# Kernel tuning notes

Measured on AMD Instinct MI355X. Metric: run time of the kernel, lower is better.

The kernel has to match this reference:

```python
import jax, jax.numpy as jnp
import numpy as np

B, S, H = 4, 2048, 768
NUM_POS = B * (S // 4)  # fixed count of positive clc_label entries (2048, even)
NEG_BIG = -1000000000.0


def setup_inputs() -> dict:
    key = jax.random.key(0)
    k1, k2, k3, k4, k5 = jax.random.split(key, 5)
    encoded_states = jax.random.normal(k1, (B, S, H), dtype=jnp.float32)
    # sorted cell-ids -> contiguous segments for the equality mask
    indicator = jnp.sort(jax.random.randint(k2, (B, S), 0, 256, dtype=jnp.int32), axis=-1)
    # clc_label: first S//4 positions per row are positive targets (class ids in [1,S)),
    # last S//2 positions are -1 (attendable keys), rest 0 (ignored)
    pos_labels = jax.random.randint(k3, (B, S // 4), 1, S, dtype=jnp.int32)
    clc_label = jnp.zeros((B, S), dtype=jnp.int32)
    clc_label = clc_label.at[:, : S // 4].set(pos_labels)
    clc_label = clc_label.at[:, S // 2:].set(-1)
    # uniform_linear params (torch Linear: y = x @ W.T + b)
    W = jax.random.normal(k4, (H, H), dtype=jnp.float32) / np.sqrt(H)
    b = jax.random.normal(k5, (H,), dtype=jnp.float32) * 0.01
    return {"encoded_states": encoded_states, "W": W, "b": b,
            "indicator": indicator, "clc_label": clc_label}


def _ce(logits, labels):
    # mean cross entropy; all labels are > 0 here so ignore_index=0 never triggers
    logp = jax.nn.log_softmax(logits, axis=-1)
    return -jnp.take_along_axis(logp, labels[:, None], axis=1).mean()


def reference(encoded_states, W, b, indicator, clc_label):
    # indicator-equality mask matmul == within-segment sum (the segment-reduce emulation)
    seg_mask = (indicator[:, :, None] == indicator[:, None, :]).astype(encoded_states.dtype)  # [B,S,S]
    agg = jnp.einsum("bij,bjh->bih", seg_mask, encoded_states)  # [B,S,H]
    # Q and K use the SAME linear on the same input -> compute once
    proj = jnp.tanh(agg @ W.T + b)  # [B,S,H]
    scores = jnp.einsum("bih,bjh->bij", proj, proj)  # [B,S,S]
    # attend only to positions where clc_label < 0
    allow = (clc_label < 0)[:, None, :]  # [B,1,S]
    scores = scores + jnp.where(allow, 0.0, NEG_BIG).astype(scores.dtype)
    flat = scores.reshape(-1, S)          # [B*S, S]
    labels = clc_label.reshape(-1)        # [B*S]
    pos_idx = jnp.nonzero(labels > 0, size=NUM_POS)[0]  # row-major order == torch bool-indexing
    logits = flat[pos_idx]                # [NUM_POS, S]
    labs = labels[pos_idx]                # [NUM_POS]
    sep_logits, sep_labels = logits[0::2], labs[0::2]
    tok_logits, tok_labels = logits[1::2], labs[1::2]
    sep_loss = _ce(sep_logits, sep_labels)
    tok_loss = _ce(tok_logits, tok_labels)
    sep_correct = jnp.sum((jnp.argmax(sep_logits, axis=-1).astype(jnp.int32) == sep_labels).astype(jnp.float32))
    tok_correct = jnp.sum((jnp.argmax(tok_logits, axis=-1).astype(jnp.int32) == tok_labels).astype(jnp.float32))
    sep_count = jnp.asarray(sep_logits.shape[0] + 1e-6, dtype=jnp.float32)
    tok_count = jnp.asarray(tok_logits.shape[0] + 1e-6, dtype=jnp.float32)
    return ((sep_loss, sep_correct, sep_count), (tok_loss, tok_correct, tok_count))
```

## Files before the change

kernel.cpp:

```cpp
#include <hip/hip_runtime.h>
#include <math.h>
#include <limits.h>

#define BB 4
#define SS 2048
#define HH 768
#define MAXSEG 256
#define NUM_POS (BB*(SS/4))
#define NEG_BIG -1000000000.0f

typedef _Float16 f16x8 __attribute__((ext_vector_type(8)));
typedef _Float16 f16x4 __attribute__((ext_vector_type(4)));
typedef float    f32x4 __attribute__((ext_vector_type(4)));

__global__ __launch_bounds__(256) void k_scanW(
    const int* __restrict__ ind, const int* __restrict__ clc,
    const float* __restrict__ W, _Float16* __restrict__ Wh,
    int* __restrict__ seg_id, int* __restrict__ seg_start,
    int* __restrict__ nseg, int* __restrict__ pos_local, int* __restrict__ pos_cnt,
    int* __restrict__ allowCnt, int* __restrict__ firstAllow)
{
  int t = threadIdx.x;
  if (blockIdx.x >= BB) {
    int idx = (blockIdx.x - BB)*256 + t;
    float4 v = ((const float4*)W)[idx];
    f16x4 h;
    h[0] = (_Float16)v.x; h[1] = (_Float16)v.y;
    h[2] = (_Float16)v.z; h[3] = (_Float16)v.w;
    *(f16x4*)(Wh + (size_t)idx*4) = h;
    return;
  }
  int b = blockIdx.x;
  int lane = t & 63, wid = t >> 6;
  __shared__ int sInd[SS];
  __shared__ int sWave[4];
  __shared__ int sAC[MAXSEG];
  __shared__ int sFA[MAXSEG];
  for (int i = t; i < SS; i += 256) sInd[i] = ind[b*SS + i];
  sAC[t] = 0; sFA[t] = INT_MAX;
  __syncthreads();

  int i0 = t * 8;
  int f[8], cv[8];
  int lsum = 0;
  #pragma unroll
  for (int u = 0; u < 8; u++) {
    int i = i0 + u;
    f[u] = (i == 0) ? 0 : (sInd[i] != sInd[i-1]);
    cv[u] = clc[b*SS + i];
    lsum += f[u];
  }
  int x = lsum;
  #pragma unroll
  for (int off = 1; off < 64; off <<= 1) {
    int v = __shfl_up(x, off, 64);
    if (lane >= off) x += v;
  }
  if (lane == 63) sWave[wid] = x;
  __syncthreads();
  int base = 0;
  for (int w = 0; w < wid; w++) base += sWave[w];
  int run = base + x - lsum;
  int rid[8];
  #pragma unroll
  for (int u = 0; u < 8; u++) {
    int i = i0 + u;
    run += f[u];
    rid[u] = run;
    seg_id[b*SS + i] = run;
    if (f[u] || i == 0) seg_start[b*(MAXSEG+1) + run] = i;
  }
  if (t == 255) { nseg[b] = run + 1; seg_start[b*(MAXSEG+1) + run + 1] = SS; }

  #pragma unroll
  for (int u = 0; u < 8; u++) {
    if (cv[u] < 0) {
      atomicAdd(&sAC[rid[u]], 1);
      atomicMin(&sFA[rid[u]], i0 + u);
    }
  }
  __syncthreads();
  allowCnt[b*MAXSEG + t]   = sAC[t];
  firstAllow[b*MAXSEG + t] = sFA[t];

  int psum = 0;
  int p[8];
  #pragma unroll
  for (int u = 0; u < 8; u++) { p[u] = (cv[u] > 0) ? 1 : 0; psum += p[u]; }
  x = psum;
  #pragma unroll
  for (int off = 1; off < 64; off <<= 1) {
    int v = __shfl_up(x, off, 64);
    if (lane >= off) x += v;
  }
  __syncthreads();
  if (lane == 63) sWave[wid] = x;
  __syncthreads();
  base = 0;
  for (int w = 0; w < wid; w++) base += sWave[w];
  int rank = base + x - psum;
  #pragma unroll
  for (int u = 0; u < 8; u++) {
    if (p[u]) { pos_local[b*SS + rank] = i0 + u; rank++; }
  }
  if (t == 255) pos_cnt[b] = rank;
}

__global__ __launch_bounds__(1024) void k_segsum(
    const float* __restrict__ es,
    const int* __restrict__ seg_start, const int* __restrict__ nseg,
    _Float16* __restrict__ segsum_h)
{
  __shared__ float sP[4][HH];
  int blk = blockIdx.x, t = threadIdx.x;
  int b = blk >> 8, s = blk & 255;
  _Float16* o = segsum_h + ((size_t)b*MAXSEG + s)*HH;
  if (s >= nseg[b]) {
    if (t < HH) o[t] = (_Float16)0.f;
    return;
  }
  int g = t >> 8, tt = t & 255;
  int st = seg_start[b*(MAXSEG+1) + s];
  int en = seg_start[b*(MAXSEG+1) + s + 1];
  int len = en - st;
  int q = (len + 3) >> 2;
  int gs = st + g*q;
  int ge = gs + q; if (ge > en) ge = en;
  const float* base = es + (size_t)b*SS*HH;
  float a0 = 0.f, a1 = 0.f, a2 = 0.f;
  float b0 = 0.f, b1 = 0.f, b2 = 0.f;
  float c0 = 0.f, c1 = 0.f, c2 = 0.f;
  float d0 = 0.f, d1 = 0.f, d2 = 0.f;
  int i = gs;
  for (; i + 4 <= ge; i += 4) {
    const float* r0 = base + (size_t)i*HH;
    const float* r1 = r0 + HH;
    const float* r2 = r1 + HH;
    const float* r3 = r2 + HH;
    a0 += r0[tt]; a1 += r0[tt+256]; a2 += r0[tt+512];
    b0 += r1[tt]; b1 += r1[tt+256]; b2 += r1[tt+512];
    c0 += r2[tt]; c1 += r2[tt+256]; c2 += r2[tt+512];
    d0 += r3[tt]; d1 += r3[tt+256]; d2 += r3[tt+512];
  }
  for (; i < ge; i++) {
    const float* r = base + (size_t)i*HH;
    a0 += r[tt]; a1 += r[tt+256]; a2 += r[tt+512];
  }
  sP[g][tt]     = (a0 + b0) + (c0 + d0);
  sP[g][tt+256] = (a1 + b1) + (c1 + d1);
  sP[g][tt+512] = (a2 + b2) + (c2 + d2);
  __syncthreads();
  if (t < HH) {
    float v = (sP[0][t] + sP[1][t]) + (sP[2][t] + sP[3][t]);
    o[t] = (_Float16)v;
  }
}

__global__ __launch_bounds__(192) void k_gemmU(
    const _Float16* __restrict__ Ah, const _Float16* __restrict__ Wh,
    const float* __restrict__ bias, _Float16* __restrict__ Uh)
{
  int tid = threadIdx.x;
  int w = tid >> 6, lane = tid & 63;
  int tile = blockIdx.x*3 + w;
  int tm = tile / 24, tn = tile % 24;
  int rb = tm*32, cb = tn*32;
  int m0 = lane & 15, quad = lane >> 4;
  const _Float16* A0 = Ah + (size_t)(rb + m0)*HH + quad*8;
  const _Float16* A1 = A0 + (size_t)16*HH;
  const _Float16* B0 = Wh + (size_t)(cb + m0)*HH + quad*8;
  const _Float16* B1 = B0 + (size_t)16*HH;
  f32x4 acc00 = {0.f,0.f,0.f,0.f}, acc01 = {0.f,0.f,0.f,0.f};
  f32x4 acc10 = {0.f,0.f,0.f,0.f}, acc11 = {0.f,0.f,0.f,0.f};
  #pragma unroll 4
  for (int k0 = 0; k0 < HH; k0 += 32) {
    f16x8 a0 = *(const f16x8*)(A0 + k0);
    f16x8 a1 = *(const f16x8*)(A1 + k0);
    f16x8 b0 = *(const f16x8*)(B0 + k0);
    f16x8 b1 = *(const f16x8*)(B1 + k0);
    acc00 = __builtin_amdgcn_mfma_f32_16x16x32_f16(a0, b0, acc00, 0, 0, 0);
    acc01 = __builtin_amdgcn_mfma_f32_16x16x32_f16(a0, b1, acc01, 0, 0, 0);
    acc10 = __builtin_amdgcn_mfma_f32_16x16x32_f16(a1, b0, acc10, 0, 0, 0);
    acc11 = __builtin_amdgcn_mfma_f32_16x16x32_f16(a1, b1, acc11, 0, 0, 0);
  }
  float bc0 = bias[cb + m0], bc1 = bias[cb + 16 + m0];
  int r0 = rb + quad*4;
  #pragma unroll
  for (int i = 0; i < 4; i++) {
    Uh[(size_t)(r0+i)*HH    + cb + m0]      = (_Float16)tanhf(acc00[i] + bc0);
    Uh[(size_t)(r0+i)*HH    + cb + 16 + m0] = (_Float16)tanhf(acc01[i] + bc1);
    Uh[(size_t)(r0+16+i)*HH + cb + m0]      = (_Float16)tanhf(acc10[i] + bc0);
    Uh[(size_t)(r0+16+i)*HH + cb + 16 + m0] = (_Float16)tanhf(acc11[i] + bc1);
  }
}

__global__ __launch_bounds__(256) void k_gram(
    const _Float16* __restrict__ Uh, float* __restrict__ G)
{
  int tid = threadIdx.x;
  int w = tid >> 6, lane = tid & 63;
  int tile = blockIdx.x*4 + w;
  int b = tile >> 8, rem = tile & 255;
  int rb = (rem >> 4)*16, cb = (rem & 15)*16;
  int m0 = lane & 15, quad = lane >> 4;
  const _Float16* Ub = Uh + (size_t)b*MAXSEG*HH;
  const _Float16* A0 = Ub + (size_t)(rb + m0)*HH + quad*8;
  const _Float16* B0 = Ub + (size_t)(cb + m0)*HH + quad*8;
  f32x4 acc = {0.f,0.f,0.f,0.f};
  #pragma unroll 4
  for (int k0 = 0; k0 < HH; k0 += 32) {
    f16x8 a  = *(const f16x8*)(A0 + k0);
    f16x8 bb = *(const f16x8*)(B0 + k0);
    acc = __builtin_amdgcn_mfma_f32_16x16x32_f16(a, bb, acc, 0, 0, 0);
  }
  float* Gb = G + (size_t)b*MAXSEG*MAXSEG;
  int r0 = rb + quad*4;
  #pragma unroll
  for (int i = 0; i < 4; i++)
    Gb[(size_t)(r0+i)*MAXSEG + cb + m0] = acc[i];
}

__global__ __launch_bounds__(256) void k_seglse(
    const float* __restrict__ G, const int* __restrict__ allowCnt,
    const int* __restrict__ firstAllow, const int* __restrict__ nseg,
    float* __restrict__ lse, int* __restrict__ amax)
{
  int lane = threadIdx.x & 63, wid = threadIdx.x >> 6;
  int row = blockIdx.x * 4 + wid;
  int b = row >> 8, si = row & 255;
  if (si >= nseg[b]) return;
  const float* g = G + ((size_t)b*MAXSEG + si)*MAXSEG;
  const int* ac = allowCnt + b*MAXSEG;
  const int* fa = firstAllow + b*MAXSEG;

  float4 gv = ((const float4*)g)[lane];
  int4   av = ((const int4*)ac)[lane];
  int4   fv = ((const int4*)fa)[lane];
  float gvv[4] = {gv.x, gv.y, gv.z, gv.w};
  int   avv[4] = {av.x, av.y, av.z, av.w};
  int   fvv[4] = {fv.x, fv.y, fv.z, fv.w};

  float m = -INFINITY;
  #pragma unroll
  for (int q = 0; q < 4; q++) if (avv[q] > 0) m = fmaxf(m, gvv[q]);
  #pragma unroll
  for (int off = 32; off > 0; off >>= 1) m = fmaxf(m, __shfl_xor(m, off, 64));
  float s = 0.f;
  #pragma unroll
  for (int q = 0; q < 4; q++) if (avv[q] > 0) s += (float)avv[q] * expf(gvv[q] - m);
  #pragma unroll
  for (int off = 32; off > 0; off >>= 1) s += __shfl_xor(s, off, 64);
  float bv = -INFINITY; int bi = INT_MAX;
  #pragma unroll
  for (int q = 0; q < 4; q++) {
    if (avv[q] > 0 && (gvv[q] > bv || (gvv[q] == bv && fvv[q] < bi))) { bv = gvv[q]; bi = fvv[q]; }
  }
  #pragma unroll
  for (int off = 32; off > 0; off >>= 1) {
    float ov = __shfl_xor(bv, off, 64);
    int   oi = __shfl_xor(bi, off, 64);
    if (ov > bv || (ov == bv && oi < bi)) { bv = ov; bi = oi; }
  }
  if (lane == 0) {
    lse[row]  = m + logf(s);
    amax[row] = bi;
  }
}

__global__ __launch_bounds__(256) void k_posfinal(
    const float* __restrict__ G, const int* __restrict__ seg_id,
    const int* __restrict__ clc, const int* __restrict__ pos_local,
    const int* __restrict__ pos_cnt, const float* __restrict__ lse,
    const int* __restrict__ amax, float* __restrict__ out)
{
  __shared__ int sBase[BB+1];
  __shared__ float sL0[4], sC0[4], sL1[4], sC1[4];
  int t = threadIdx.x;
  if (t == 0) {
    int acc = 0; sBase[0] = 0;
    for (int b = 0; b < BB; b++) { acc += pos_cnt[b]; sBase[b+1] = acc; }
  }
  __syncthreads();
  int total = sBase[BB];
  if (total > NUM_POS) total = NUM_POS;

  int rs[8]; bool ok[8]; int bv[8];
  #pragma unroll
  for (int u = 0; u < 8; u++) {
    rs[u] = t + 256*u;
    ok[u] = rs[u] < total;
    int b = 0;
    if (ok[u]) { while (b < BB-1 && rs[u] >= sBase[b+1]) b++; }
    bv[u] = b;
  }
  int iv[8];
  #pragma unroll
  for (int u = 0; u < 8; u++)
    iv[u] = ok[u] ? pos_local[bv[u]*SS + (rs[u] - sBase[bv[u]])] : 0;
  int Lv[8], sv[8];
  #pragma unroll
  for (int u = 0; u < 8; u++) {
    Lv[u] = ok[u] ? clc[bv[u]*SS + iv[u]] : 0;
    sv[u] = ok[u] ? seg_id[bv[u]*SS + iv[u]] : 0;
  }
  int sLv[8], cLv[8];
  #pragma unroll
  for (int u = 0; u < 8; u++) {
    sLv[u] = ok[u] ? seg_id[bv[u]*SS + Lv[u]] : 0;
    cLv[u] = ok[u] ? clc[bv[u]*SS + Lv[u]] : 0;
  }
  float gv[8], lv[8]; int av[8];
  #pragma unroll
  for (int u = 0; u < 8; u++) {
    gv[u] = ok[u] ? G[((size_t)bv[u]*MAXSEG + sv[u])*MAXSEG + sLv[u]] : 0.f;
    lv[u] = ok[u] ? lse[bv[u]*MAXSEG + sv[u]] : 0.f;
    av[u] = ok[u] ? amax[bv[u]*MAXSEG + sv[u]] : -1;
  }

  float l0 = 0.f, c0 = 0.f, l1 = 0.f, c1 = 0.f;
  #pragma unroll
  for (int u = 0; u < 8; u++) {
    if (!ok[u]) continue;
    float vL = gv[u] + (cLv[u] < 0 ? 0.0f : NEG_BIG);
    float loss = lv[u] - vL;
    float corr = (av[u] == Lv[u]) ? 1.0f : 0.0f;
    if (rs[u] & 1) { l1 += loss; c1 += corr; } else { l0 += loss; c0 += corr; }
  }

  int lane = t & 63, wid = t >> 6;
  #pragma unroll
  for (int off = 32; off > 0; off >>= 1) {
    l0 += __shfl_down(l0, off, 64);
    c0 += __shfl_down(c0, off, 64);
    l1 += __shfl_down(l1, off, 64);
    c1 += __shfl_down(c1, off, 64);
  }
  if (lane == 0) { sL0[wid] = l0; sC0[wid] = c0; sL1[wid] = l1; sC1[wid] = c1; }
  __syncthreads();
  if (t == 0) {
    float L0 = sL0[0]+sL0[1]+sL0[2]+sL0[3];
    float C0 = sC0[0]+sC0[1]+sC0[2]+sC0[3];
    float L1 = sL1[0]+sL1[1]+sL1[2]+sL1[3];
    float C1 = sC1[0]+sC1[1]+sC1[2]+sC1[3];
    float n = (float)(NUM_POS/2);
    out[0] = L0 / n;
    out[1] = C0;
    out[2] = n + 1e-6f;
    out[3] = L1 / n;
    out[4] = C1;
    out[5] = n + 1e-6f;
  }
}

extern "C" void kernel_launch(void* const* d_in, const int* in_sizes, int n_in,
                              void* d_out, int out_size, void* d_ws, size_t ws_size,
                              hipStream_t stream)
{
  const float* es   = (const float*)d_in[0];
  const float* W    = (const float*)d_in[1];
  const float* bias = (const float*)d_in[2];
  const int*   ind  = (const int*)d_in[3];
  const int*   clc  = (const int*)d_in[4];
  float* out = (float*)d_out;

  char* ws = (char*)d_ws;
  int*   nseg       = (int*)(ws + 0);
  int*   pos_cnt    = (int*)(ws + 256);
  int*   seg_start  = (int*)(ws + 1024);
  int*   seg_id     = (int*)(ws + 8192);
  int*   pos_local  = (int*)(ws + 40960);
  int*   allowCnt   = (int*)(ws + 73728);
  int*   firstAllow = (int*)(ws + 77824);
  float* lse        = (float*)(ws + 81920);
  int*   amax       = (int*)(ws + 86016);
  _Float16* segsum_h = (_Float16*)(ws + 90112);
  _Float16* Wh       = (_Float16*)(ws + 1662976);
  _Float16* Uh       = (_Float16*)(ws + 2842624);
  float*    G        = (float*)(ws + 4415488);

  k_scanW<<<BB + 576, 256, 0, stream>>>(ind, clc, W, Wh, seg_id, seg_start,
                                        nseg, pos_local, pos_cnt, allowCnt, firstAllow);
  k_segsum<<<BB*MAXSEG, 1024, 0, stream>>>(es, seg_start, nseg, segsum_h);
  k_gemmU<<<256, 192, 0, stream>>>(segsum_h, Wh, bias, Uh);
  k_gram<<<256, 256, 0, stream>>>(Uh, G);
  k_seglse<<<(BB*MAXSEG)/4, 256, 0, stream>>>(G, allowCnt, firstAllow, nseg, lse, amax);
  k_posfinal<<<1, 256, 0, stream>>>(G, seg_id, clc, pos_local, pos_cnt, lse, amax, out);
}
```

Baseline: 117.4 us.

## Fuse gram and segment LSE kernels and precompute positive-row records in scan

Merges the Gram-matrix MFMA kernel with the per-segment log-sum-exp/argmax kernel. Each 1024-thread block computes a 16-row stripe of G into shared memory and reduces it in place, which removes one launch and the reload of G from global memory. The scan kernel also stages clc and segment ids in LDS and writes a packed int4 record per positive row (segment, label segment, label, label clc). This replaces the chain of dependent gathers in the single-block final kernel with one load. The trade-off is that the fused kernel launches only 64 blocks instead of 256, so fewer CUs do the Gram work.

New measurement: 130.7 us. 11.3% more time.

```diff
diff --git a/kernel.cpp b/kernel.cpp
--- a/kernel.cpp
+++ b/kernel.cpp
@@ -7,6 +7,7 @@
 #define HH 768
 #define MAXSEG 256
 #define NUM_POS (BB*(SS/4))
+#define PPB (SS/4)
 #define NEG_BIG -1000000000.0f
 
 typedef _Float16 f16x8 __attribute__((ext_vector_type(8)));
@@ -16,8 +17,8 @@
 __global__ __launch_bounds__(256) void k_scanW(
     const int* __restrict__ ind, const int* __restrict__ clc,
     const float* __restrict__ W, _Float16* __restrict__ Wh,
-    int* __restrict__ seg_id, int* __restrict__ seg_start,
-    int* __restrict__ nseg, int* __restrict__ pos_local, int* __restrict__ pos_cnt,
+    int* __restrict__ seg_start, int* __restrict__ nseg,
+    int4* __restrict__ pos_rec, int* __restrict__ pos_cnt,
     int* __restrict__ allowCnt, int* __restrict__ firstAllow)
 {
   int t = threadIdx.x;
@@ -33,10 +34,15 @@
   int b = blockIdx.x;
   int lane = t & 63, wid = t >> 6;
   __shared__ int sInd[SS];
+  __shared__ int sClc[SS];
+  __shared__ int sSeg[SS];
   __shared__ int sWave[4];
   __shared__ int sAC[MAXSEG];
   __shared__ int sFA[MAXSEG];
-  for (int i = t; i < SS; i += 256) sInd[i] = ind[b*SS + i];
+  for (int i = t; i < SS/4; i += 256) {
+    ((int4*)sInd)[i] = ((const int4*)(ind + b*SS))[i];
+    ((int4*)sClc)[i] = ((const int4*)(clc + b*SS))[i];
+  }
   sAC[t] = 0; sFA[t] = INT_MAX;
   __syncthreads();
 
@@ -47,7 +53,7 @@
   for (int u = 0; u < 8; u++) {
     int i = i0 + u;
     f[u] = (i == 0) ? 0 : (sInd[i] != sInd[i-1]);
-    cv[u] = clc[b*SS + i];
+    cv[u] = sClc[i];
     lsum += f[u];
   }
   int x = lsum;
@@ -67,7 +73,7 @@
     int i = i0 + u;
     run += f[u];
     rid[u] = run;
-    seg_id[b*SS + i] = run;
+    sSeg[i] = run;
     if (f[u] || i == 0) seg_start[b*(MAXSEG+1) + run] = i;
   }
   if (t == 255) { nseg[b] = run + 1; seg_start[b*(MAXSEG+1) + run + 1] = SS; }
@@ -101,7 +107,16 @@
   int rank = base + x - psum;
   #pragma unroll
   for (int u = 0; u < 8; u++) {
-    if (p[u]) { pos_local[b*SS + rank] = i0 + u; rank++; }
+    if (p[u]) {
+      int L = cv[u];
+      int4 rec;
+      rec.x = rid[u];
+      rec.y = sSeg[L];
+      rec.z = L;
+      rec.w = sClc[L];
+      pos_rec[b*PPB + rank] = rec;
+      rank++;
+    }
   }
   if (t == 255) pos_cnt[b] = rank;
 }
@@ -194,17 +209,21 @@
   }
 }
 
-__global__ __launch_bounds__(256) void k_gram(
-    const _Float16* __restrict__ Uh, float* __restrict__ G)
-{
-  int tid = threadIdx.x;
-  int w = tid >> 6, lane = tid & 63;
-  int tile = blockIdx.x*4 + w;
-  int b = tile >> 8, rem = tile & 255;
-  int rb = (rem >> 4)*16, cb = (rem & 15)*16;
+__global__ __launch_bounds__(1024) void k_gramlse(
+    const _Float16* __restrict__ Uh, const int* __restrict__ allowCnt,
+    const int* __restrict__ firstAllow, const int* __restrict__ nseg,
+    float* __restrict__ G, float* __restrict__ lse, int* __restrict__ amax)
+{
+  __shared__ float sG[16][257];
+  int t = threadIdx.x;
+  int lane = t & 63, w = t >> 6;
+  int blk = blockIdx.x;
+  int b = blk >> 4;
+  int rb = (blk & 15) * 16;
   int m0 = lane & 15, quad = lane >> 4;
   const _Float16* Ub = Uh + (size_t)b*MAXSEG*HH;
   const _Float16* A0 = Ub + (size_t)(rb + m0)*HH + quad*8;
+  int cb = w * 16;
   const _Float16* B0 = Ub + (size_t)(cb + m0)*HH + quad*8;
   f32x4 acc = {0.f,0.f,0.f,0.f};
   #pragma unroll 4
@@ -214,46 +233,38 @@
     acc = __builtin_amdgcn_mfma_f32_16x16x32_f16(a, bb, acc, 0, 0, 0);
   }
   float* Gb = G + (size_t)b*MAXSEG*MAXSEG;
-  int r0 = rb + quad*4;
-  #pragma unroll
-  for (int i = 0; i < 4; i++)
-    Gb[(size_t)(r0+i)*MAXSEG + cb + m0] = acc[i];
-}
-
-__global__ __launch_bounds__(256) void k_seglse(
-    const float* __restrict__ G, const int* __restrict__ allowCnt,
-    const int* __restrict__ firstAllow, const int* __restrict__ nseg,
-    float* __restrict__ lse, int* __restrict__ amax)
-{
-  int lane = threadIdx.x & 63, wid = threadIdx.x >> 6;
-  int row = blockIdx.x * 4 + wid;
-  int b = row >> 8, si = row & 255;
+  int r0 = quad*4;
+  #pragma unroll
+  for (int i = 0; i < 4; i++) {
+    sG[r0 + i][cb + m0] = acc[i];
+    Gb[(size_t)(rb + r0 + i)*MAXSEG + cb + m0] = acc[i];
+  }
+  __syncthreads();
+
+  int si = rb + w;
   if (si >= nseg[b]) return;
-  const float* g = G + ((size_t)b*MAXSEG + si)*MAXSEG;
   const int* ac = allowCnt + b*MAXSEG;
   const int* fa = firstAllow + b*MAXSEG;
-
-  float4 gv = ((const float4*)g)[lane];
-  int4   av = ((const int4*)ac)[lane];
-  int4   fv = ((const int4*)fa)[lane];
-  float gvv[4] = {gv.x, gv.y, gv.z, gv.w};
-  int   avv[4] = {av.x, av.y, av.z, av.w};
-  int   fvv[4] = {fv.x, fv.y, fv.z, fv.w};
-
+  float gv[4]; int av[4], fv[4];
+  #pragma unroll
+  for (int q = 0; q < 4; q++) {
+    int s = lane + 64*q;
+    gv[q] = sG[w][s]; av[q] = ac[s]; fv[q] = fa[s];
+  }
   float m = -INFINITY;
   #pragma unroll
-  for (int q = 0; q < 4; q++) if (avv[q] > 0) m = fmaxf(m, gvv[q]);
+  for (int q = 0; q < 4; q++) if (av[q] > 0) m = fmaxf(m, gv[q]);
   #pragma unroll
   for (int off = 32; off > 0; off >>= 1) m = fmaxf(m, __shfl_xor(m, off, 64));
   float s = 0.f;
   #pragma unroll
-  for (int q = 0; q < 4; q++) if (avv[q] > 0) s += (float)avv[q] * expf(gvv[q] - m);
+  for (int q = 0; q < 4; q++) if (av[q] > 0) s += (float)av[q] * expf(gv[q] - m);
   #pragma unroll
   for (int off = 32; off > 0; off >>= 1) s += __shfl_xor(s, off, 64);
   float bv = -INFINITY; int bi = INT_MAX;
   #pragma unroll
   for (int q = 0; q < 4; q++) {
-    if (avv[q] > 0 && (gvv[q] > bv || (gvv[q] == bv && fvv[q] < bi))) { bv = gvv[q]; bi = fvv[q]; }
+    if (av[q] > 0 && (gv[q] > bv || (gv[q] == bv && fv[q] < bi))) { bv = gv[q]; bi = fv[q]; }
   }
   #pragma unroll
   for (int off = 32; off > 0; off >>= 1) {
@@ -262,14 +273,13 @@
     if (ov > bv || (ov == bv && oi < bi)) { bv = ov; bi = oi; }
   }
   if (lane == 0) {
-    lse[row]  = m + logf(s);
-    amax[row] = bi;
+    lse[b*MAXSEG + si]  = m + logf(s);
+    amax[b*MAXSEG + si] = bi;
   }
 }
 
 __global__ __launch_bounds__(256) void k_posfinal(
-    const float* __restrict__ G, const int* __restrict__ seg_id,
-    const int* __restrict__ clc, const int* __restrict__ pos_local,
+    const float* __restrict__ G, const int4* __restrict__ pos_rec,
     const int* __restrict__ pos_cnt, const float* __restrict__ lse,
     const int* __restrict__ amax, float* __restrict__ out)
 {
@@ -293,37 +303,27 @@
     if (ok[u]) { while (b < BB-1 && rs[u] >= sBase[b+1]) b++; }
     bv[u] = b;
   }
-  int iv[8];
-  #pragma unroll
-  for (int u = 0; u < 8; u++)
-    iv[u] = ok[u] ? pos_local[bv[u]*SS + (rs[u] - sBase[bv[u]])] : 0;
-  int Lv[8], sv[8];
-  #pragma unroll
-  for (int u = 0; u < 8; u++) {
-    Lv[u] = ok[u] ? clc[bv[u]*SS + iv[u]] : 0;
-    sv[u] = ok[u] ? seg_id[bv[u]*SS + iv[u]] : 0;
-  }
-  int sLv[8], cLv[8];
-  #pragma unroll
-  for (int u = 0; u < 8; u++) {
-    sLv[u] = ok[u] ? seg_id[bv[u]*SS + Lv[u]] : 0;
-    cLv[u] = ok[u] ? clc[bv[u]*SS + Lv[u]] : 0;
+  int4 rec[8];
+  #pragma unroll
+  for (int u = 0; u < 8; u++) {
+    rec[u] = ok[u] ? pos_rec[bv[u]*PPB + (rs[u] - sBase[bv[u]])]
+                   : make_int4(0, 0, 0, 0);
   }
   float gv[8], lv[8]; int av[8];
   #pragma unroll
   for (int u = 0; u < 8; u++) {
-    gv[u] = ok[u] ? G[((size_t)bv[u]*MAXSEG + sv[u])*MAXSEG + sLv[u]] : 0.f;
-    lv[u] = ok[u] ? lse[bv[u]*MAXSEG + sv[u]] : 0.f;
-    av[u] = ok[u] ? amax[bv[u]*MAXSEG + sv[u]] : -1;
+    gv[u] = ok[u] ? G[((size_t)bv[u]*MAXSEG + rec[u].x)*MAXSEG + rec[u].y] : 0.f;
+    lv[u] = ok[u] ? lse[bv[u]*MAXSEG + rec[u].x] : 0.f;
+    av[u] = ok[u] ? amax[bv[u]*MAXSEG + rec[u].x] : -1;
   }
 
   float l0 = 0.f, c0 = 0.f, l1 = 0.f, c1 = 0.f;
   #pragma unroll
   for (int u = 0; u < 8; u++) {
     if (!ok[u]) continue;
-    float vL = gv[u] + (cLv[u] < 0 ? 0.0f : NEG_BIG);
+    float vL = gv[u] + (rec[u].w < 0 ? 0.0f : NEG_BIG);
     float loss = lv[u] - vL;
-    float corr = (av[u] == Lv[u]) ? 1.0f : 0.0f;
+    float corr = (av[u] == rec[u].z) ? 1.0f : 0.0f;
     if (rs[u] & 1) { l1 += loss; c1 += corr; } else { l0 += loss; c0 += corr; }
   }
 
@@ -367,8 +367,7 @@
   int*   nseg       = (int*)(ws + 0);
   int*   pos_cnt    = (int*)(ws + 256);
   int*   seg_start  = (int*)(ws + 1024);
-  int*   seg_id     = (int*)(ws + 8192);
-  int*   pos_local  = (int*)(ws + 40960);
+  int4*  pos_rec    = (int4*)(ws + 40960);
   int*   allowCnt   = (int*)(ws + 73728);
   int*   firstAllow = (int*)(ws + 77824);
   float* lse        = (float*)(ws + 81920);
@@ -378,11 +377,10 @@
   _Float16* Uh       = (_Float16*)(ws + 2842624);
   float*    G        = (float*)(ws + 4415488);
 
-  k_scanW<<<BB + 576, 256, 0, stream>>>(ind, clc, W, Wh, seg_id, seg_start,
-                                        nseg, pos_local, pos_cnt, allowCnt, firstAllow);
+  k_scanW<<<BB + 576, 256, 0, stream>>>(ind, clc, W, Wh, seg_start,
+                                        nseg, pos_rec, pos_cnt, allowCnt, firstAllow);
   k_segsum<<<BB*MAXSEG, 1024, 0, stream>>>(es, seg_start, nseg, segsum_h);
   k_gemmU<<<256, 192, 0, stream>>>(segsum_h, Wh, bias, Uh);
-  k_gram<<<256, 256, 0, stream>>>(Uh, G);
-  k_seglse<<<(BB*MAXSEG)/4, 256, 0, stream>>>(G, allowCnt, firstAllow, nseg, lse, amax);
-  k_posfinal<<<1, 256, 0, stream>>>(G, seg_id, clc, pos_local, pos_cnt, lse, amax, out);
-}
+  k_gramlse<<<BB*16, 1024, 0, stream>>>(Uh, allowCnt, firstAllow, nseg, G, lse, amax);
+  k_posfinal<<<1, 256, 0, stream>>>(G, pos_rec, pos_cnt, lse, amax, out);
+}
```
